# Kernel tuning notes

Hardware: AMD Instinct MI355X
Metric: run time of the kernel (lower is better)

Reference implementation:

```python
import jax, jax.numpy as jnp
import numpy as np

N_NODES = 50000
N_EDGES = 800000
HID = 128


def setup_inputs() -> dict:
    key = jax.random.key(0)
    ks = jax.random.split(key, 8)
    h = jax.random.normal(ks[0], (N_NODES, HID), dtype=jnp.float32)
    edge_index = jax.random.randint(ks[1], (2, N_EDGES), 0, N_NODES, dtype=jnp.int64)
    edge_attr = jax.random.normal(ks[2], (N_EDGES, HID), dtype=jnp.float32)
    # MLP params: Linear(3H -> H), Linear(H -> 1). Stored as [in, out] so y = x @ W + b.
    s1 = 1.0 / np.sqrt(3 * HID)
    W1 = jax.random.uniform(ks[3], (3 * HID, HID), minval=-s1, maxval=s1, dtype=jnp.float32)
    b1 = jax.random.uniform(ks[4], (HID,), minval=-s1, maxval=s1, dtype=jnp.float32)
    s2 = 1.0 / np.sqrt(HID)
    W2 = jax.random.uniform(ks[5], (HID, 1), minval=-s2, maxval=s2, dtype=jnp.float32)
    b2 = jax.random.uniform(ks[6], (1,), minval=-s2, maxval=s2, dtype=jnp.float32)
    return {"h": h, "edge_index": edge_index, "edge_attr": edge_attr,
            "W1": W1, "b1": b1, "W2": W2, "b2": b2}


def reference(h, edge_index, edge_attr, W1, b1, W2, b2):
    row, col = edge_index[0], edge_index[1]
    h_i = h[row]                      # [E, H] gather of source nodes
    h_j = h[col]                      # [E, H] gather of target nodes
    # Split first Linear over the concat [h_i, h_j, edge_attr] to avoid a [E, 3H] buffer.
    Wa, Wb, Wc = W1[:HID], W1[HID:2 * HID], W1[2 * HID:]
    pre = h_i @ Wa + h_j @ Wb + edge_attr @ Wc + b1      # [E, H]
    a = jax.nn.elu(pre) @ W2 + b2                        # [E, 1]
    a = jax.nn.leaky_relu(a, negative_slope=0.2)
    alpha = jax.nn.softmax(a, axis=0)                    # softmax over all edges (dim=0)
    h_agg = jnp.zeros_like(h).at[row].add(alpha * h_j)   # scatter-add weighted neighbors
    return h_agg
```

## Files before the change

### kernel.cpp

```cpp
#include <hip/hip_runtime.h>
#include <hip/hip_bf16.h>
#include <math.h>

#define NNODES 50000
#define NEDGES 800000
#define HID    128
#define NB_SCAN 196
#define NB_EDGE 6250

typedef short bf16x8 __attribute__((ext_vector_type(8)));
typedef float f32x4  __attribute__((ext_vector_type(4)));

__device__ __forceinline__ unsigned short bf16_rn(float x) {
    union { float f; unsigned int u; } v; v.f = x;
    unsigned int r = v.u + 0x7fffu + ((v.u >> 16) & 1u);
    return (unsigned short)(r >> 16);
}
__device__ __forceinline__ float bf16_to_f(unsigned short u) {
    union { unsigned int u; float f; } v; v.u = ((unsigned int)u) << 16;
    return v.f;
}

__device__ __forceinline__ float expm1_fast(float x) {
    float t = 1.9841270e-4f;
    t = fmaf(t, x, 1.3888889e-3f);
    t = fmaf(t, x, 8.3333333e-3f);
    t = fmaf(t, x, 4.1666668e-2f);
    t = fmaf(t, x, 0.16666667f);
    t = fmaf(t, x, 0.5f);
    t = fmaf(t, x, 1.0f);
    float poly = x * t;
    float ex   = __expf(x) - 1.0f;
    return (x > -0.25f) ? poly : ex;
}

__global__ void k_prep(const float* __restrict__ W1, unsigned short* __restrict__ Wt)
{
    const float* Wc = W1 + 256 * 128;
    int base = (blockIdx.x * 256 + threadIdx.x) * 4;
#pragma unroll
    for (int i = 0; i < 4; ++i) {
        int idx = base + i;
        int c = idx >> 7, k = idx & 127;
        Wt[c * 128 + k] = bf16_rn(Wc[k * 128 + c]);
    }
}

__global__ __launch_bounds__(256) void k_gemm_node(
    const float* __restrict__ h, const float* __restrict__ W1,
    const float* __restrict__ b1, unsigned short* __restrict__ Hab)
{
    __shared__ float at[32][132];
    __shared__ float bt[32][128];

    const int tid = threadIdx.x;
    const int tx  = tid & 15;
    const int ty  = tid >> 4;
    const int nb  = blockIdx.x * 128;
    const int by  = blockIdx.y;
    const float* W = W1 + by * 128 * 128;

    float acc[8][8];
#pragma unroll
    for (int j = 0; j < 8; ++j)
#pragma unroll
        for (int c = 0; c < 8; ++c) acc[j][c] = 0.0f;

    for (int ks = 0; ks < 128; ks += 32) {
#pragma unroll
        for (int p = 0; p < 16; ++p) {
            int i  = (tid >> 5) + p * 8;
            int kk = tid & 31;
            int n  = nb + i;
            at[kk][i] = (n < NNODES) ? h[n * 128 + ks + kk] : 0.0f;
        }
#pragma unroll
        for (int p = 0; p < 16; ++p) {
            int kk = (tid >> 7) + p * 2;
            int c  = tid & 127;
            bt[kk][c] = W[(ks + kk) * 128 + c];
        }
        __syncthreads();
#pragma unroll
        for (int k = 0; k < 32; ++k) {
            float av[8], bv[8];
            *(float4*)&av[0] = *(const float4*)&at[k][ty * 8];
            *(float4*)&av[4] = *(const float4*)&at[k][ty * 8 + 4];
            *(float4*)&bv[0] = *(const float4*)&bt[k][tx * 8];
            *(float4*)&bv[4] = *(const float4*)&bt[k][tx * 8 + 4];
#pragma unroll
            for (int j = 0; j < 8; ++j)
#pragma unroll
                for (int c = 0; c < 8; ++c)
                    acc[j][c] = fmaf(av[j], bv[c], acc[j][c]);
        }
        __syncthreads();
    }

    float b1v[8];
    if (by == 0) {
        *(float4*)&b1v[0] = *(const float4*)&b1[tx * 8];
        *(float4*)&b1v[4] = *(const float4*)&b1[tx * 8 + 4];
    } else {
#pragma unroll
        for (int c = 0; c < 8; ++c) b1v[c] = 0.0f;
    }
#pragma unroll
    for (int j = 0; j < 8; ++j) {
        int n = nb + ty * 8 + j;
        if (n < NNODES) {
            unsigned short o[8];
#pragma unroll
            for (int c = 0; c < 8; ++c) o[c] = bf16_rn(acc[j][c] + b1v[c]);
            unsigned short* dst = Hab + (size_t)n * 256 + by * 128 + tx * 8;
            *(int4*)dst = *(int4*)&o[0];
        }
    }
}

__global__ __launch_bounds__(256) void k_edge_mfma(
    const float* __restrict__ ea, const int* __restrict__ eidx,
    const unsigned short* __restrict__ Wt, const float* __restrict__ W2,
    const float* __restrict__ b2, const unsigned short* __restrict__ Hab,
    float* __restrict__ a_out, int* __restrict__ hist,
    float* __restrict__ bmax, float* __restrict__ bsumE)
{
    const int tid  = threadIdx.x;
    const int w    = tid >> 6;
    const int l    = tid & 63;
    const int quad = l >> 4;
    const int lm   = l & 15;
    const int wm   = w * 32;
    const int ebase = blockIdx.x * 128;

    __shared__ float sred[8];

    f32x4 acc[2][8] = {};

    int rows0[4], cols0[4], rows1[4], cols1[4];
    {
        const int e40 = ebase + wm + quad * 4;
        const int e41 = e40 + 16;
#pragma unroll
        for (int r = 0; r < 4; ++r) {
            rows0[r] = eidx[e40 + r];
            cols0[r] = eidx[NEDGES + e40 + r];
            rows1[r] = eidx[e41 + r];
            cols1[r] = eidx[NEDGES + e41 + r];
        }
    }
    if (lm == 0) {
#pragma unroll
        for (int r = 0; r < 4; ++r) {
            atomicAdd(&hist[rows0[r]], 1);
            atomicAdd(&hist[rows1[r]], 1);
        }
    }

    const float* abase0 = ea + (size_t)(ebase + wm + lm) * 128 + quad * 8;
    const float* abase1 = abase0 + 16 * 128;
    float4 raw[2][2][2];
    raw[0][0][0] = *(const float4*)(abase0);
    raw[0][0][1] = *(const float4*)(abase0 + 4);
    raw[0][1][0] = *(const float4*)(abase1);
    raw[0][1][1] = *(const float4*)(abase1 + 4);

    bf16x8 hav[2][4], hbv[2][4];

#pragma unroll
    for (int stage = 0; stage < 4; ++stage) {
        const int ks  = stage * 32;
        const int cur = stage & 1, nxt = cur ^ 1;
        if (stage < 3) {
            const int ko = ks + 32;
            raw[nxt][0][0] = *(const float4*)(abase0 + ko);
            raw[nxt][0][1] = *(const float4*)(abase0 + ko + 4);
            raw[nxt][1][0] = *(const float4*)(abase1 + ko);
            raw[nxt][1][1] = *(const float4*)(abase1 + ko + 4);
        }
        if (stage == 3) {
#pragma unroll
            for (int r = 0; r < 4; ++r) {
                hav[0][r] = *(const bf16x8*)(Hab + (size_t)rows0[r] * 256 + lm * 8);
                hbv[0][r] = *(const bf16x8*)(Hab + (size_t)cols0[r] * 256 + 128 + lm * 8);
                hav[1][r] = *(const bf16x8*)(Hab + (size_t)rows1[r] * 256 + lm * 8);
                hbv[1][r] = *(const bf16x8*)(Hab + (size_t)cols1[r] * 256 + 128 + lm * 8);
            }
        }
        bf16x8 bfrag[8];
#pragma unroll
        for (int nt = 0; nt < 8; ++nt) {
            const unsigned short* bp = Wt + (lm * 8 + nt) * 128 + ks + quad * 8;
            bfrag[nt] = *(const bf16x8*)bp;
        }
        bf16x8 afrag[2];
#pragma unroll
        for (int mt = 0; mt < 2; ++mt) {
            float4 x0 = raw[cur][mt][0];
            float4 x1 = raw[cur][mt][1];
            bf16x8 f;
            f[0] = (short)bf16_rn(x0.x); f[1] = (short)bf16_rn(x0.y);
            f[2] = (short)bf16_rn(x0.z); f[3] = (short)bf16_rn(x0.w);
            f[4] = (short)bf16_rn(x1.x); f[5] = (short)bf16_rn(x1.y);
            f[6] = (short)bf16_rn(x1.z); f[7] = (short)bf16_rn(x1.w);
            afrag[mt] = f;
        }
#pragma unroll
        for (int mt = 0; mt < 2; ++mt)
#pragma unroll
            for (int nt = 0; nt < 8; ++nt)
                acc[mt][nt] = __builtin_amdgcn_mfma_f32_16x16x32_bf16(
                    afrag[mt], bfrag[nt], acc[mt][nt], 0, 0, 0);
    }

    float w2v[8];
    *(float4*)&w2v[0] = *(const float4*)&W2[lm * 8];
    *(float4*)&w2v[4] = *(const float4*)&W2[lm * 8 + 4];
    const float b2s = b2[0];

    float avl[2] = { -INFINITY, -INFINITY };

#pragma unroll
    for (int mt = 0; mt < 2; ++mt) {
        const int e4 = ebase + wm + mt * 16 + quad * 4;

        float s0 = 0.f, s1 = 0.f, s2 = 0.f, s3 = 0.f;
#pragma unroll
        for (int r = 0; r < 4; ++r) {
            float sr = 0.f;
#pragma unroll
            for (int nt = 0; nt < 8; ++nt) {
                float ha  = bf16_to_f((unsigned short)hav[mt][r][nt]);
                float hb  = bf16_to_f((unsigned short)hbv[mt][r][nt]);
                float pre = acc[mt][nt][r] + ha + hb;
                float el  = pre > 0.f ? pre : expm1_fast(pre);
                sr = fmaf(el, w2v[nt], sr);
            }
            if (r == 0) s0 = sr; else if (r == 1) s1 = sr; else if (r == 2) s2 = sr; else s3 = sr;
        }
#pragma unroll
        for (int m = 1; m < 16; m <<= 1) {
            s0 += __shfl_xor(s0, m, 64);
            s1 += __shfl_xor(s1, m, 64);
            s2 += __shfl_xor(s2, m, 64);
            s3 += __shfl_xor(s3, m, 64);
        }
        if (lm < 4) {
            float sum = (lm == 0) ? s0 : (lm == 1) ? s1 : (lm == 2) ? s2 : s3;
            sum += b2s;
            float av = sum >= 0.f ? sum : 0.2f * sum;
            a_out[e4 + lm] = av;
            avl[mt] = av;
        }
    }

    float m = fmaxf(avl[0], avl[1]);
#pragma unroll
    for (int msk = 1; msk < 64; msk <<= 1) m = fmaxf(m, __shfl_xor(m, msk, 64));
    if (l == 0) sred[w] = m;
    __syncthreads();
    float mb = fmaxf(fmaxf(sred[0], sred[1]), fmaxf(sred[2], sred[3]));
    float es = 0.f;
    if (avl[0] > -INFINITY)
        es = expf(avl[0] - mb) + expf(avl[1] - mb);
#pragma unroll
    for (int msk = 1; msk < 64; msk <<= 1) es += __shfl_xor(es, msk, 64);
    if (l == 0) sred[4 + w] = es;
    __syncthreads();
    if (tid == 0) {
        bmax[blockIdx.x]  = mb;
        bsumE[blockIdx.x] = sred[4] + sred[5] + sred[6] + sred[7];
    }
}

__global__ void k_scan_blk(const int* __restrict__ hist, int* __restrict__ offsets,
                           int* __restrict__ bsum)
{
    __shared__ int sd[256];
    int t = threadIdx.x, i = blockIdx.x * 256 + t;
    int v = (i < NNODES) ? hist[i] : 0;
    sd[t] = v; __syncthreads();
    for (int off = 1; off < 256; off <<= 1) {
        int add = (t >= off) ? sd[t - off] : 0;
        __syncthreads();
        sd[t] += add;
        __syncthreads();
    }
    if (i < NNODES) offsets[i] = sd[t] - v;
    if (t == 255) bsum[blockIdx.x] = sd[255];
}

__global__ void k_scan_top(const int* __restrict__ bsum, int* __restrict__ bpre,
                           int* __restrict__ offsets)
{
    __shared__ int sd[256];
    int t = threadIdx.x;
    int v = (t < NB_SCAN) ? bsum[t] : 0;
    sd[t] = v; __syncthreads();
    for (int off = 1; off < 256; off <<= 1) {
        int add = (t >= off) ? sd[t - off] : 0;
        __syncthreads();
        sd[t] += add;
        __syncthreads();
    }
    if (t < NB_SCAN) bpre[t] = sd[t] - v;
    if (t == 255) offsets[NNODES] = sd[255];
}

__global__ void k_scan_add(int* __restrict__ offsets, const int* __restrict__ bpre)
{
    int i = blockIdx.x * 256 + threadIdx.x;
    if (i < NNODES) offsets[i] += bpre[i >> 8];
}

__global__ void k_scatter(const int* __restrict__ eidx, const int* __restrict__ offsets,
                          int* __restrict__ cursor, int2* __restrict__ pairs)
{
    int e = blockIdx.x * 256 + threadIdx.x;
    if (e < NEDGES) {
        int r   = eidx[e];
        int pos = offsets[r] + atomicAdd(&cursor[r], 1);
        pairs[pos] = make_int2(e, eidx[NEDGES + e]);
    }
}

__global__ __launch_bounds__(1024) void k_final(
    const float* __restrict__ bmax, const float* __restrict__ bsumE,
    float* __restrict__ mz)
{
    __shared__ float sd[1024];
    int tid = threadIdx.x;
    float m = -INFINITY;
    for (int i = tid; i < NB_EDGE; i += 1024) m = fmaxf(m, bmax[i]);
    sd[tid] = m; __syncthreads();
    for (int off = 512; off > 0; off >>= 1) {
        if (tid < off) sd[tid] = fmaxf(sd[tid], sd[tid + off]);
        __syncthreads();
    }
    float M = sd[0];
    __syncthreads();
    float s = 0.f;
    for (int i = tid; i < NB_EDGE; i += 1024) s += bsumE[i] * expf(bmax[i] - M);
    sd[tid] = s; __syncthreads();
    for (int off = 512; off > 0; off >>= 1) {
        if (tid < off) sd[tid] += sd[tid + off];
        __syncthreads();
    }
    if (tid == 0) { mz[0] = M; mz[1] = 1.0f / sd[0]; }
}

__global__ __launch_bounds__(256) void k_agg(
    const float* __restrict__ h, const float* __restrict__ a,
    const int2* __restrict__ pairs, const int* __restrict__ offsets,
    const float* __restrict__ mz, float* __restrict__ out)
{
    int node = blockIdx.x * 4 + (threadIdx.x >> 6);
    int lane = threadIdx.x & 63;
    if (node >= NNODES) return;
    const float M    = mz[0];
    const float invS = mz[1];
    int s0 = offsets[node], s1 = offsets[node + 1];
    float2 acc = make_float2(0.0f, 0.0f);
    int i = s0;
    for (; i + 8 <= s1; i += 8) {
        int2 p[8];
#pragma unroll
        for (int r = 0; r < 8; ++r) p[r] = pairs[i + r];
        float av[8];
#pragma unroll
        for (int r = 0; r < 8; ++r) av[r] = a[p[r].x];
        float2 hv[8];
#pragma unroll
        for (int r = 0; r < 8; ++r)
            hv[r] = *(const float2*)(h + (size_t)p[r].y * 128 + lane * 2);
#pragma unroll
        for (int r = 0; r < 8; ++r) {
            float al = expf(av[r] - M) * invS;
            acc.x = fmaf(al, hv[r].x, acc.x);
            acc.y = fmaf(al, hv[r].y, acc.y);
        }
    }
    for (; i < s1; ++i) {
        int2 p = pairs[i];
        float al = expf(a[p.x] - M) * invS;
        float2 hj = *(const float2*)(h + (size_t)p.y * 128 + lane * 2);
        acc.x = fmaf(al, hj.x, acc.x);
        acc.y = fmaf(al, hj.y, acc.y);
    }
    *(float2*)(out + (size_t)node * 128 + lane * 2) = acc;
}

extern "C" void kernel_launch(void* const* d_in, const int* in_sizes, int n_in,
                              void* d_out, int out_size, void* d_ws, size_t ws_size,
                              hipStream_t stream)
{
    const float* h    = (const float*)d_in[0];
    const int*   eidx = (const int*)d_in[1];
    const float* ea   = (const float*)d_in[2];
    const float* W1   = (const float*)d_in[3];
    const float* b1   = (const float*)d_in[4];
    const float* W2   = (const float*)d_in[5];
    const float* b2   = (const float*)d_in[6];
    float* out = (float*)d_out;

    char* ws = (char*)d_ws;
    unsigned short* Hab = (unsigned short*)(ws);
    float* a_arr   = (float*)(ws + 25600000);
    int2*  pairs   = (int2*) (ws + 28800000);
    int*   offsets = (int*)  (ws + 35200000);
    int*   cursor  = (int*)  (ws + 35400192);
    float* bmax    = (float*)(ws + 35600384);
    float* bsumE   = (float*)(ws + 35625984);
    float* mz      = (float*)(ws + 35651584);
    unsigned short* Wt = (unsigned short*)(ws + 35651648);
    int*   bsum_s  = (int*)  (ws + 35684416);
    int*   bpre_s  = (int*)  (ws + 35685440);

    hipMemsetAsync(cursor, 0, NNODES * sizeof(int), stream);

    k_prep<<<16, 256, 0, stream>>>(W1, Wt);
    k_gemm_node<<<dim3((NNODES + 127) / 128, 2), 256, 0, stream>>>(h, W1, b1, Hab);

    k_edge_mfma<<<NB_EDGE, 256, 0, stream>>>(ea, eidx, Wt, W2, b2, Hab,
                                             a_arr, cursor, bmax, bsumE);

    k_scan_blk<<<NB_SCAN, 256, 0, stream>>>(cursor, offsets, bsum_s);
    k_scan_top<<<1, 256, 0, stream>>>(bsum_s, bpre_s, offsets);
    k_scan_add<<<NB_SCAN, 256, 0, stream>>>(offsets, bpre_s);
    hipMemsetAsync(cursor, 0, NNODES * sizeof(int), stream);
    k_scatter<<<(NEDGES + 255) / 256, 256, 0, stream>>>(eidx, offsets, cursor, pairs);

    k_final<<<1, 1024, 0, stream>>>(bmax, bsumE, mz);
    k_agg<<<(NNODES + 3) / 4, 256, 0, stream>>>(h, a_arr, pairs, offsets, mz, out);
}
```

Measured before the change: 869.2 us.

## Stage W tile in swizzled LDS, vectorize index loads, precompute alpha in scatter

The edge MFMA kernel now copies the 128x128 bf16 weight matrix into XOR-swizzled shared memory once per block and reads B fragments from LDS instead of global memory. Edge indices are loaded as int4 vectors. The softmax weight is computed in the scatter kernel, which now runs after k_final, and stored in the pairs array, so the aggregation kernel no longer does a random gather of a[] or an exp per edge. In exchange each block uses 32KB of LDS, which may reduce occupancy, and every block reloads W into LDS.

```diff
diff --git a/kernel.cpp b/kernel.cpp
--- a/kernel.cpp
+++ b/kernel.cpp
@@ -133,7 +133,17 @@
     const int wm   = w * 32;
     const int ebase = blockIdx.x * 128;
 
+    __shared__ __align__(16) unsigned short wlds[16384];
     __shared__ float sred[8];
+
+#pragma unroll
+    for (int i = 0; i < 8; ++i) {
+        int idx16 = i * 2048 + tid * 8;
+        int c = idx16 >> 7;
+        bf16x8 v = *(const bf16x8*)(Wt + idx16);
+        int byte = (idx16 * 2) ^ (((c >> 3) & 15) << 4);
+        *(bf16x8*)((char*)wlds + byte) = v;
+    }
 
     f32x4 acc[2][8] = {};
 
@@ -141,13 +151,14 @@
     {
         const int e40 = ebase + wm + quad * 4;
         const int e41 = e40 + 16;
-#pragma unroll
-        for (int r = 0; r < 4; ++r) {
-            rows0[r] = eidx[e40 + r];
-            cols0[r] = eidx[NEDGES + e40 + r];
-            rows1[r] = eidx[e41 + r];
-            cols1[r] = eidx[NEDGES + e41 + r];
-        }
+        int4 r0 = *(const int4*)(eidx + e40);
+        int4 c0 = *(const int4*)(eidx + NEDGES + e40);
+        int4 r1 = *(const int4*)(eidx + e41);
+        int4 c1 = *(const int4*)(eidx + NEDGES + e41);
+        rows0[0] = r0.x; rows0[1] = r0.y; rows0[2] = r0.z; rows0[3] = r0.w;
+        cols0[0] = c0.x; cols0[1] = c0.y; cols0[2] = c0.z; cols0[3] = c0.w;
+        rows1[0] = r1.x; rows1[1] = r1.y; rows1[2] = r1.z; rows1[3] = r1.w;
+        cols1[0] = c1.x; cols1[1] = c1.y; cols1[2] = c1.z; cols1[3] = c1.w;
     }
     if (lm == 0) {
 #pragma unroll
@@ -166,6 +177,8 @@
     raw[0][1][1] = *(const float4*)(abase1 + 4);
 
     bf16x8 hav[2][4], hbv[2][4];
+
+    __syncthreads();
 
 #pragma unroll
     for (int stage = 0; stage < 4; ++stage) {
@@ -190,8 +203,9 @@
         bf16x8 bfrag[8];
 #pragma unroll
         for (int nt = 0; nt < 8; ++nt) {
-            const unsigned short* bp = Wt + (lm * 8 + nt) * 128 + ks + quad * 8;
-            bfrag[nt] = *(const bf16x8*)bp;
+            const int c = lm * 8 + nt;
+            const int byte = (c * 256 + (ks + quad * 8) * 2) ^ ((lm & 15) << 4);
+            bfrag[nt] = *(const bf16x8*)((const char*)wlds + byte);
         }
         bf16x8 afrag[2];
 #pragma unroll
@@ -313,17 +327,6 @@
     if (i < NNODES) offsets[i] += bpre[i >> 8];
 }
 
-__global__ void k_scatter(const int* __restrict__ eidx, const int* __restrict__ offsets,
-                          int* __restrict__ cursor, int2* __restrict__ pairs)
-{
-    int e = blockIdx.x * 256 + threadIdx.x;
-    if (e < NEDGES) {
-        int r   = eidx[e];
-        int pos = offsets[r] + atomicAdd(&cursor[r], 1);
-        pairs[pos] = make_int2(e, eidx[NEDGES + e]);
-    }
-}
-
 __global__ __launch_bounds__(1024) void k_final(
     const float* __restrict__ bmax, const float* __restrict__ bsumE,
     float* __restrict__ mz)
@@ -349,16 +352,26 @@
     if (tid == 0) { mz[0] = M; mz[1] = 1.0f / sd[0]; }
 }
 
+__global__ void k_scatter(const int* __restrict__ eidx, const int* __restrict__ offsets,
+                          int* __restrict__ cursor, const float* __restrict__ a,
+                          const float* __restrict__ mz, int2* __restrict__ pairs)
+{
+    int e = blockIdx.x * 256 + threadIdx.x;
+    if (e < NEDGES) {
+        int r    = eidx[e];
+        float al = expf(a[e] - mz[0]) * mz[1];
+        int pos  = offsets[r] + atomicAdd(&cursor[r], 1);
+        pairs[pos] = make_int2(__float_as_int(al), eidx[NEDGES + e]);
+    }
+}
+
 __global__ __launch_bounds__(256) void k_agg(
-    const float* __restrict__ h, const float* __restrict__ a,
-    const int2* __restrict__ pairs, const int* __restrict__ offsets,
-    const float* __restrict__ mz, float* __restrict__ out)
+    const float* __restrict__ h, const int2* __restrict__ pairs,
+    const int* __restrict__ offsets, float* __restrict__ out)
 {
     int node = blockIdx.x * 4 + (threadIdx.x >> 6);
     int lane = threadIdx.x & 63;
     if (node >= NNODES) return;
-    const float M    = mz[0];
-    const float invS = mz[1];
     int s0 = offsets[node], s1 = offsets[node + 1];
     float2 acc = make_float2(0.0f, 0.0f);
     int i = s0;
@@ -366,23 +379,20 @@
         int2 p[8];
 #pragma unroll
         for (int r = 0; r < 8; ++r) p[r] = pairs[i + r];
-        float av[8];
-#pragma unroll
-        for (int r = 0; r < 8; ++r) av[r] = a[p[r].x];
         float2 hv[8];
 #pragma unroll
         for (int r = 0; r < 8; ++r)
             hv[r] = *(const float2*)(h + (size_t)p[r].y * 128 + lane * 2);
 #pragma unroll
         for (int r = 0; r < 8; ++r) {
-            float al = expf(av[r] - M) * invS;
+            float al = __int_as_float(p[r].x);
             acc.x = fmaf(al, hv[r].x, acc.x);
             acc.y = fmaf(al, hv[r].y, acc.y);
         }
     }
     for (; i < s1; ++i) {
         int2 p = pairs[i];
-        float al = expf(a[p.x] - M) * invS;
+        float al = __int_as_float(p.x);
         float2 hj = *(const float2*)(h + (size_t)p.y * 128 + lane * 2);
         acc.x = fmaf(al, hj.x, acc.x);
         acc.y = fmaf(al, hj.y, acc.y);
@@ -428,8 +438,9 @@
     k_scan_top<<<1, 256, 0, stream>>>(bsum_s, bpre_s, offsets);
     k_scan_add<<<NB_SCAN, 256, 0, stream>>>(offsets, bpre_s);
     hipMemsetAsync(cursor, 0, NNODES * sizeof(int), stream);
-    k_scatter<<<(NEDGES + 255) / 256, 256, 0, stream>>>(eidx, offsets, cursor, pairs);
 
     k_final<<<1, 1024, 0, stream>>>(bmax, bsumE, mz);
-    k_agg<<<(NNODES + 3) / 4, 256, 0, stream>>>(h, a_arr, pairs, offsets, mz, out);
-}
+    k_scatter<<<(NEDGES + 255) / 256, 256, 0, stream>>>(eidx, offsets, cursor,
+                                                        a_arr, mz, pairs);
+    k_agg<<<(NNODES + 3) / 4, 256, 0, stream>>>(h, pairs, offsets, out);
+}
```

Result: faster. 803.5 us (-7.6%).
